# Performance work log

Hardware: AMD Instinct MI355X
Metric: run time of the kernel (lower is better)

The kernel has to match this reference:

```python
import jax, jax.numpy as jnp
import numpy as np

B, S_REF, E, H = 128, 2048, 512, 512

def setup_inputs() -> dict:
    key = jax.random.key(0)
    ks = jax.random.split(key, 13)
    def lin(kw, kb, out_d, in_d):
        bound = 1.0 / np.sqrt(in_d)
        w = jax.random.uniform(kw, (out_d, in_d), minval=-bound, maxval=bound, dtype=jnp.float32)
        b = jax.random.uniform(kb, (out_d,), minval=-bound, maxval=bound, dtype=jnp.float32)
        return w, b
    Wa_w, Wa_b = lin(ks[0], ks[1], H, H)
    Ua_w, Ua_b = lin(ks[2], ks[3], H, H)
    Va_w, Va_b = lin(ks[4], ks[5], 1, H)
    Wih_w, Wih_b = lin(ks[6], ks[7], H, E + H)
    Whh_w, Whh_b = lin(ks[8], ks[9], H, H)
    x_t = jax.random.normal(ks[10], (B, 1, E), dtype=jnp.float32)
    x_ref_encoded = jax.random.normal(ks[11], (B, S_REF, H), dtype=jnp.float32)
    h_prev = jax.random.normal(ks[12], (B, H), dtype=jnp.float32)
    return {"x_t": x_t, "x_ref_encoded": x_ref_encoded, "h_prev": h_prev,
            "Wa_w": Wa_w, "Wa_b": Wa_b, "Ua_w": Ua_w, "Ua_b": Ua_b,
            "Va_w": Va_w, "Va_b": Va_b, "Wih_w": Wih_w, "Wih_b": Wih_b,
            "Whh_w": Whh_w, "Whh_b": Whh_b}

def reference(x_t, x_ref_encoded, h_prev, Wa_w, Wa_b, Ua_w, Ua_b, Va_w, Va_b, Wih_w, Wih_b, Whh_w, Whh_b):
    # Bahdanau additive attention
    q = h_prev @ Wa_w.T + Wa_b                      # (B, H)
    k = jnp.einsum('bsh,oh->bso', x_ref_encoded, Ua_w) + Ua_b  # (B, S, H)
    scores = jnp.einsum('bsh,h->bs', jnp.tanh(q[:, None, :] + k), Va_w[0]) + Va_b[0]  # (B, S)
    attn_weights = jax.nn.softmax(scores, axis=1)
    context = jnp.einsum('bs,bsh->bh', attn_weights, x_ref_encoded)  # (B, H)
    # Reservoir RNN cell on concat(x_t[:,0,:], context)
    rnn_in = jnp.concatenate([x_t[:, 0, :], context], axis=1)        # (B, E+H)
    h_next = jnp.tanh(rnn_in @ Wih_w.T + Wih_b + h_prev @ Whh_w.T + Whh_b)
    return (h_next, context)
```

## Files before the change

### kernel.cpp

```cpp
#include <hip/hip_runtime.h>
#include <hip/hip_bf16.h>
#include <math.h>


typedef __attribute__((ext_vector_type(8))) short short8;
typedef __attribute__((ext_vector_type(8))) unsigned short ushort8;
typedef __attribute__((ext_vector_type(4))) float f32x4;

#define S_LEN 2048
#define BDIM 128
#define HDIM 512
#define EDIM 512
#define BM 64
#define NCHUNK (S_LEN / BM)

__device__ __forceinline__ unsigned short f2bf(float f) {
  unsigned int u = __float_as_uint(f);
  u += 0x7fffu + ((u >> 16) & 1u);
  return (unsigned short)(u >> 16);
}

__device__ __forceinline__ float bf2f(unsigned short u) {
  return __uint_as_float(((unsigned int)u) << 16);
}

__device__ __forceinline__ float fast_tanh(float x) {
  float e = __expf(2.0f * x);
  return 1.0f - 2.0f / (e + 1.0f);
}

__global__ __launch_bounds__(256) void k_cvt_b(const float* __restrict__ src,
                                               unsigned short* __restrict__ dst) {
  int tid = blockIdx.x * 256 + threadIdx.x;
  int ct = tid >> 10;
  int kt = (tid >> 6) & 15;
  int l = tid & 63;
  int col = ct * 16 + (l & 15);
  int k = kt * 32 + (l >> 4) * 8;
  const float4* s = (const float4*)(src + (size_t)col * HDIM + k);
  float4 v0 = s[0], v1 = s[1];
  ushort8 p;
  p[0] = f2bf(v0.x); p[1] = f2bf(v0.y); p[2] = f2bf(v0.z); p[3] = f2bf(v0.w);
  p[4] = f2bf(v1.x); p[5] = f2bf(v1.y); p[6] = f2bf(v1.z); p[7] = f2bf(v1.w);
  *(ushort8*)(dst + (size_t)tid * 8) = p;
}

__global__ __launch_bounds__(256) void k_q(const float* __restrict__ hp,
                                           const float* __restrict__ Wa,
                                           const float* __restrict__ Wab,
                                           const float* __restrict__ Uab,
                                           float* __restrict__ q) {
  int b = blockIdx.x, oh = blockIdx.y;
  int o = oh * 256 + threadIdx.x;
  __shared__ float hs[HDIM];
  hs[threadIdx.x] = hp[b * HDIM + threadIdx.x];
  hs[threadIdx.x + 256] = hp[b * HDIM + threadIdx.x + 256];
  __syncthreads();
  const float4* wr = (const float4*)(Wa + (size_t)o * HDIM);
  float acc = 0.f;
#pragma unroll 8
  for (int i = 0; i < HDIM / 4; ++i) {
    float4 v = wr[i];
    acc += v.x * hs[i * 4 + 0] + v.y * hs[i * 4 + 1] + v.z * hs[i * 4 + 2] + v.w * hs[i * 4 + 3];
  }
  q[b * HDIM + o] = acc + Wab[o] + Uab[o];
}

__global__ __launch_bounds__(512, 4) void k_scores_ctx(
    const float* __restrict__ xref, const unsigned short* __restrict__ uab,
    const float* __restrict__ q, const float* __restrict__ va,
    float* __restrict__ mArr, float* __restrict__ lArr, float* __restrict__ cpart) {
  int chunk = blockIdx.x;
  int b = blockIdx.y;
  int tid = threadIdx.x;
  int l = tid & 63;
  int w = tid >> 6;
  int c = l & 15, g4 = l >> 4;

  __shared__ __align__(16) unsigned short As[BM * HDIM];
  __shared__ float sc[BM];
  __shared__ float pl[BM];

  f32x4 acc[4][2];
#pragma unroll
  for (int m = 0; m < 4; ++m)
#pragma unroll
    for (int n = 0; n < 2; ++n) acc[m][n] = f32x4{0.f, 0.f, 0.f, 0.f};

  const float* xb = xref + ((size_t)b * S_LEN + (size_t)chunk * BM) * HDIM;

  int srow = tid >> 3;
  int sk8 = (tid & 7) * 64;
  int sw = (srow & 7) << 4;
  char* wbase = (char*)&As[0] + srow * 1024;
  float4 ga0, ga1, ga2, ga3, gb0, gb1, gb2, gb3;

#define ISSUE(v0, v1, v2, v3, call)                                            \
  {                                                                            \
    const float4* gp_ = (const float4*)(xb + (size_t)srow * HDIM + sk8 + (call) * 16); \
    v0 = gp_[0]; v1 = gp_[1]; v2 = gp_[2]; v3 = gp_[3];                        \
  }

#define WRITE(v0, v1, v2, v3, call)                                            \
  {                                                                            \
    union { __hip_bfloat162 h[4]; ushort8 s; } u0_, u1_;                       \
    u0_.h[0] = __float22bfloat162_rn(make_float2(v0.x, v0.y));                 \
    u0_.h[1] = __float22bfloat162_rn(make_float2(v0.z, v0.w));                 \
    u0_.h[2] = __float22bfloat162_rn(make_float2(v1.x, v1.y));                 \
    u0_.h[3] = __float22bfloat162_rn(make_float2(v1.z, v1.w));                 \
    u1_.h[0] = __float22bfloat162_rn(make_float2(v2.x, v2.y));                 \
    u1_.h[1] = __float22bfloat162_rn(make_float2(v2.z, v2.w));                 \
    u1_.h[2] = __float22bfloat162_rn(make_float2(v3.x, v3.y));                 \
    u1_.h[3] = __float22bfloat162_rn(make_float2(v3.z, v3.w));                 \
    int kb0_ = (tid & 7) * 128 + (call) * 32;                                  \
    *(ushort8*)(wbase + (kb0_ ^ sw)) = u0_.s;                                  \
    *(ushort8*)(wbase + ((kb0_ + 16) ^ sw)) = u1_.s;                           \
  }

#define CLUSTER(h, kt)                                                         \
  {                                                                            \
    short8 afr_[4], bfr_[2];                                                   \
    _Pragma("unroll")                                                          \
    for (int n = 0; n < 2; ++n) {                                              \
      int ct = (h) * 16 + w * 2 + n;                                           \
      bfr_[n] = *(const short8*)(uab + (((size_t)(ct * 16 + (kt)) * 64 + l) * 8)); \
    }                                                                          \
    _Pragma("unroll")                                                          \
    for (int m = 0; m < 4; ++m) {                                              \
      int row = m * 16 + (l & 15);                                             \
      int kb = ((kt) * 64 + (l >> 4) * 16) ^ ((row & 7) << 4);                 \
      afr_[m] = *(const short8*)((const char*)&As[0] + row * 1024 + kb);       \
    }                                                                          \
    __builtin_amdgcn_s_setprio(1);                                             \
    _Pragma("unroll")                                                          \
    for (int m = 0; m < 4; ++m)                                                \
      _Pragma("unroll")                                                        \
      for (int n = 0; n < 2; ++n)                                              \
        acc[m][n] = __builtin_amdgcn_mfma_f32_16x16x32_bf16(afr_[m], bfr_[n],  \
                                                            acc[m][n], 0, 0, 0); \
    __builtin_amdgcn_s_setprio(0);                                             \
  }

#define EPILOGUE(qf0_, qf1_, vf0_, vf1_)                                       \
  {                                                                            \
    _Pragma("unroll")                                                          \
    for (int m = 0; m < 4; ++m) {                                              \
      _Pragma("unroll")                                                        \
      for (int r = 0; r < 4; ++r) {                                            \
        float sum = fast_tanh(acc[m][0][r] + qf0_) * vf0_ +                    \
                    fast_tanh(acc[m][1][r] + qf1_) * vf1_;                     \
        sum += __shfl_xor(sum, 1);                                             \
        sum += __shfl_xor(sum, 2);                                             \
        sum += __shfl_xor(sum, 4);                                             \
        sum += __shfl_xor(sum, 8);                                             \
        if (c == 0) atomicAdd(&sc[m * 16 + g4 * 4 + r], sum);                  \
      }                                                                        \
    }                                                                          \
  }

  ISSUE(ga0, ga1, ga2, ga3, 0); ISSUE(gb0, gb1, gb2, gb3, 1);
  WRITE(ga0, ga1, ga2, ga3, 0); ISSUE(ga0, ga1, ga2, ga3, 2);
  WRITE(gb0, gb1, gb2, gb3, 1); ISSUE(gb0, gb1, gb2, gb3, 3);
  WRITE(ga0, ga1, ga2, ga3, 2); WRITE(gb0, gb1, gb2, gb3, 3);
  if (tid < BM) sc[tid] = 0.f;
  __syncthreads();

  {
    int o0 = w * 32 + c, o1 = w * 32 + 16 + c;
    float qf0 = q[b * HDIM + o0], qf1 = q[b * HDIM + o1];
    float vf0 = va[o0], vf1 = va[o1];
    CLUSTER(0, 0)  CLUSTER(0, 1)  CLUSTER(0, 2)  CLUSTER(0, 3)
    CLUSTER(0, 4)  CLUSTER(0, 5)  CLUSTER(0, 6)  CLUSTER(0, 7)
    CLUSTER(0, 8)  CLUSTER(0, 9)  CLUSTER(0, 10) CLUSTER(0, 11)
    CLUSTER(0, 12) CLUSTER(0, 13) CLUSTER(0, 14) CLUSTER(0, 15)
    EPILOGUE(qf0, qf1, vf0, vf1)
  }

#pragma unroll
  for (int m = 0; m < 4; ++m)
#pragma unroll
    for (int n = 0; n < 2; ++n) acc[m][n] = f32x4{0.f, 0.f, 0.f, 0.f};

  {
    int o0 = 256 + w * 32 + c, o1 = 256 + w * 32 + 16 + c;
    float qf0 = q[b * HDIM + o0], qf1 = q[b * HDIM + o1];
    float vf0 = va[o0], vf1 = va[o1];
    CLUSTER(1, 0)  CLUSTER(1, 1)  CLUSTER(1, 2)  CLUSTER(1, 3)
    CLUSTER(1, 4)  CLUSTER(1, 5)  CLUSTER(1, 6)  CLUSTER(1, 7)
    CLUSTER(1, 8)  CLUSTER(1, 9)  CLUSTER(1, 10) CLUSTER(1, 11)
    CLUSTER(1, 12) CLUSTER(1, 13) CLUSTER(1, 14) CLUSTER(1, 15)
    EPILOGUE(qf0, qf1, vf0, vf1)
  }
  __syncthreads();

  float M = sc[l];
#pragma unroll
  for (int off = 32; off >= 1; off >>= 1) M = fmaxf(M, __shfl_xor(M, off));
  float pp = __expf(sc[l] - M);
  float lsum = pp;
#pragma unroll
  for (int off = 32; off >= 1; off >>= 1) lsum += __shfl_xor(lsum, off);
  if (tid < BM) pl[tid] = pp;
  if (tid == 0) {
    mArr[b * NCHUNK + chunk] = M;
    lArr[b * NCHUNK + chunk] = lsum;
  }
  __syncthreads();

  {
    int h2 = tid * 2;
    const char* base_ = (const char*)&As[0];
    float cacc = 0.f;
#pragma unroll 8
    for (int r = 0; r < BM; ++r) {
      int byte = r * 1024 + (h2 ^ ((r & 7) << 4));
      cacc += pl[r] * bf2f(*(const unsigned short*)(base_ + byte));
    }
    cpart[((size_t)b * NCHUNK + chunk) * HDIM + tid] = cacc;
  }
#undef ISSUE
#undef WRITE
#undef CLUSTER
#undef EPILOGUE
}

__global__ __launch_bounds__(512) void k_combine(const float* __restrict__ mArr,
                                                 const float* __restrict__ lArr,
                                                 const float* __restrict__ cpart,
                                                 float* __restrict__ ctx,
                                                 float* __restrict__ out_ctx) {
  int b = blockIdx.x, t = threadIdx.x;
  __shared__ float wf[NCHUNK];
  __shared__ float dinv;
  if (t == 0) {
    float M = mArr[b * NCHUNK];
    for (int i = 1; i < NCHUNK; ++i) M = fmaxf(M, mArr[b * NCHUNK + i]);
    float den = 0.f;
    for (int i = 0; i < NCHUNK; ++i) {
      float f = __expf(mArr[b * NCHUNK + i] - M);
      wf[i] = f;
      den += f * lArr[b * NCHUNK + i];
    }
    dinv = 1.0f / den;
  }
  __syncthreads();
  float s = 0.f;
#pragma unroll
  for (int i = 0; i < NCHUNK; ++i) s += wf[i] * cpart[((size_t)b * NCHUNK + i) * HDIM + t];
  float c = s * dinv;
  ctx[b * HDIM + t] = c;
  out_ctx[b * HDIM + t] = c;
}

__global__ __launch_bounds__(256) void k_rnn(const float* __restrict__ xt,
                                             const float* __restrict__ ctx,
                                             const float* __restrict__ hp,
                                             const float* __restrict__ Wih,
                                             const float* __restrict__ Wihb,
                                             const float* __restrict__ Whh,
                                             const float* __restrict__ Whhb,
                                             float* __restrict__ hout) {
  int b = blockIdx.x, oh = blockIdx.y;
  int o = oh * 256 + threadIdx.x;
  __shared__ float xs[EDIM], cs[HDIM], hs[HDIM];
  xs[threadIdx.x] = xt[b * EDIM + threadIdx.x];
  xs[threadIdx.x + 256] = xt[b * EDIM + threadIdx.x + 256];
  cs[threadIdx.x] = ctx[b * HDIM + threadIdx.x];
  cs[threadIdx.x + 256] = ctx[b * HDIM + threadIdx.x + 256];
  hs[threadIdx.x] = hp[b * HDIM + threadIdx.x];
  hs[threadIdx.x + 256] = hp[b * HDIM + threadIdx.x + 256];
  __syncthreads();
  const float4* wi = (const float4*)(Wih + (size_t)o * (EDIM + HDIM));
  float acc = Wihb[o] + Whhb[o];
#pragma unroll 8
  for (int i = 0; i < EDIM / 4; ++i) {
    float4 v = wi[i];
    acc += v.x * xs[i * 4] + v.y * xs[i * 4 + 1] + v.z * xs[i * 4 + 2] + v.w * xs[i * 4 + 3];
  }
  const float4* wi2 = wi + EDIM / 4;
#pragma unroll 8
  for (int i = 0; i < HDIM / 4; ++i) {
    float4 v = wi2[i];
    acc += v.x * cs[i * 4] + v.y * cs[i * 4 + 1] + v.z * cs[i * 4 + 2] + v.w * cs[i * 4 + 3];
  }
  const float4* wh = (const float4*)(Whh + (size_t)o * HDIM);
#pragma unroll 8
  for (int i = 0; i < HDIM / 4; ++i) {
    float4 v = wh[i];
    acc += v.x * hs[i * 4] + v.y * hs[i * 4 + 1] + v.z * hs[i * 4 + 2] + v.w * hs[i * 4 + 3];
  }
  hout[b * HDIM + o] = tanhf(acc);
}

extern "C" void kernel_launch(void* const* d_in, const int* in_sizes, int n_in,
                              void* d_out, int out_size, void* d_ws, size_t ws_size,
                              hipStream_t stream) {
  const float* x_t    = (const float*)d_in[0];
  const float* x_ref  = (const float*)d_in[1];
  const float* h_prev = (const float*)d_in[2];
  const float* Wa_w   = (const float*)d_in[3];
  const float* Wa_b   = (const float*)d_in[4];
  const float* Ua_w   = (const float*)d_in[5];
  const float* Ua_b   = (const float*)d_in[6];
  const float* Va_w   = (const float*)d_in[7];
  const float* Wih_w  = (const float*)d_in[9];
  const float* Wih_b  = (const float*)d_in[10];
  const float* Whh_w  = (const float*)d_in[11];
  const float* Whh_b  = (const float*)d_in[12];

  char* ws = (char*)d_ws;
  unsigned short* ua_fr = (unsigned short*)ws;
  float* q     = (float*)(ws + 524288);
  float* mArr  = (float*)(ws + 786432);
  float* lArr  = (float*)(ws + 802816);
  float* cpart = (float*)(ws + 819200);
  float* ctx   = (float*)(ws + 9207808);

  float* h_out   = (float*)d_out;
  float* ctx_out = h_out + BDIM * HDIM;

  k_cvt_b<<<dim3(128), dim3(256), 0, stream>>>(Ua_w, ua_fr);
  k_q<<<dim3(BDIM, 2), dim3(256), 0, stream>>>(h_prev, Wa_w, Wa_b, Ua_b, q);
  k_scores_ctx<<<dim3(NCHUNK, BDIM), dim3(512), 0, stream>>>(x_ref, ua_fr, q, Va_w, mArr, lArr, cpart);
  k_combine<<<dim3(BDIM), dim3(512), 0, stream>>>(mArr, lArr, cpart, ctx, ctx_out);
  k_rnn<<<dim3(BDIM, 2), dim3(256), 0, stream>>>(x_t, ctx, h_prev, Wih_w, Wih_b, Whh_w, Whh_b, h_out);
}
```

Before: 350.4 us.

## Widen MFMA N-tile to four per wave and single-pass score epilogue

Result: faster. 294.9 us (-15.8%).

```diff
diff --git a/kernel.cpp b/kernel.cpp
--- a/kernel.cpp
+++ b/kernel.cpp
@@ -81,48 +81,42 @@
   __shared__ float sc[BM];
   __shared__ float pl[BM];
 
-  f32x4 acc[4][2];
+  f32x4 acc[4][4];
 #pragma unroll
   for (int m = 0; m < 4; ++m)
 #pragma unroll
-    for (int n = 0; n < 2; ++n) acc[m][n] = f32x4{0.f, 0.f, 0.f, 0.f};
+    for (int n = 0; n < 4; ++n) acc[m][n] = f32x4{0.f, 0.f, 0.f, 0.f};
 
   const float* xb = xref + ((size_t)b * S_LEN + (size_t)chunk * BM) * HDIM;
 
-  int srow = tid >> 3;
-  int sk8 = (tid & 7) * 64;
-  int sw = (srow & 7) << 4;
-  char* wbase = (char*)&As[0] + srow * 1024;
-  float4 ga0, ga1, ga2, ga3, gb0, gb1, gb2, gb3;
-
-#define ISSUE(v0, v1, v2, v3, call)                                            \
+  int srow = tid >> 3, skq = tid & 7;
+  char* wb = (char*)&As[0] + srow * 1024 + ((skq * 16) ^ ((srow & 7) << 4));
+  const float* sb = xb + (size_t)srow * HDIM + skq * 8;
+
+  float4 a0, a1, a2, a3, a4, a5, a6, a7;
+
+#define LD2(va, vb, p)                                                         \
   {                                                                            \
-    const float4* gp_ = (const float4*)(xb + (size_t)srow * HDIM + sk8 + (call) * 16); \
-    v0 = gp_[0]; v1 = gp_[1]; v2 = gp_[2]; v3 = gp_[3];                        \
-  }
-
-#define WRITE(v0, v1, v2, v3, call)                                            \
+    va = *(const float4*)(sb + (p) * 64);                                      \
+    vb = *(const float4*)(sb + (p) * 64 + 4);                                  \
+  }
+
+#define WR1(va, vb, p)                                                         \
   {                                                                            \
-    union { __hip_bfloat162 h[4]; ushort8 s; } u0_, u1_;                       \
-    u0_.h[0] = __float22bfloat162_rn(make_float2(v0.x, v0.y));                 \
-    u0_.h[1] = __float22bfloat162_rn(make_float2(v0.z, v0.w));                 \
-    u0_.h[2] = __float22bfloat162_rn(make_float2(v1.x, v1.y));                 \
-    u0_.h[3] = __float22bfloat162_rn(make_float2(v1.z, v1.w));                 \
-    u1_.h[0] = __float22bfloat162_rn(make_float2(v2.x, v2.y));                 \
-    u1_.h[1] = __float22bfloat162_rn(make_float2(v2.z, v2.w));                 \
-    u1_.h[2] = __float22bfloat162_rn(make_float2(v3.x, v3.y));                 \
-    u1_.h[3] = __float22bfloat162_rn(make_float2(v3.z, v3.w));                 \
-    int kb0_ = (tid & 7) * 128 + (call) * 32;                                  \
-    *(ushort8*)(wbase + (kb0_ ^ sw)) = u0_.s;                                  \
-    *(ushort8*)(wbase + ((kb0_ + 16) ^ sw)) = u1_.s;                           \
-  }
-
-#define CLUSTER(h, kt)                                                         \
+    union { __hip_bfloat162 h[4]; ushort8 s; } u_;                             \
+    u_.h[0] = __float22bfloat162_rn(make_float2(va.x, va.y));                  \
+    u_.h[1] = __float22bfloat162_rn(make_float2(va.z, va.w));                  \
+    u_.h[2] = __float22bfloat162_rn(make_float2(vb.x, vb.y));                  \
+    u_.h[3] = __float22bfloat162_rn(make_float2(vb.z, vb.w));                  \
+    *(ushort8*)(wb + (p) * 128) = u_.s;                                        \
+  }
+
+#define CLUSTER(kt)                                                            \
   {                                                                            \
-    short8 afr_[4], bfr_[2];                                                   \
+    short8 afr_[4], bfr_[4];                                                   \
     _Pragma("unroll")                                                          \
-    for (int n = 0; n < 2; ++n) {                                              \
-      int ct = (h) * 16 + w * 2 + n;                                           \
+    for (int n = 0; n < 4; ++n) {                                              \
+      int ct = w * 4 + n;                                                      \
       bfr_[n] = *(const short8*)(uab + (((size_t)(ct * 16 + (kt)) * 64 + l) * 8)); \
     }                                                                          \
     _Pragma("unroll")                                                          \
@@ -135,61 +129,46 @@
     _Pragma("unroll")                                                          \
     for (int m = 0; m < 4; ++m)                                                \
       _Pragma("unroll")                                                        \
-      for (int n = 0; n < 2; ++n)                                              \
+      for (int n = 0; n < 4; ++n)                                              \
         acc[m][n] = __builtin_amdgcn_mfma_f32_16x16x32_bf16(afr_[m], bfr_[n],  \
                                                             acc[m][n], 0, 0, 0); \
     __builtin_amdgcn_s_setprio(0);                                             \
   }
 
-#define EPILOGUE(qf0_, qf1_, vf0_, vf1_)                                       \
-  {                                                                            \
-    _Pragma("unroll")                                                          \
-    for (int m = 0; m < 4; ++m) {                                              \
-      _Pragma("unroll")                                                        \
-      for (int r = 0; r < 4; ++r) {                                            \
-        float sum = fast_tanh(acc[m][0][r] + qf0_) * vf0_ +                    \
-                    fast_tanh(acc[m][1][r] + qf1_) * vf1_;                     \
-        sum += __shfl_xor(sum, 1);                                             \
-        sum += __shfl_xor(sum, 2);                                             \
-        sum += __shfl_xor(sum, 4);                                             \
-        sum += __shfl_xor(sum, 8);                                             \
-        if (c == 0) atomicAdd(&sc[m * 16 + g4 * 4 + r], sum);                  \
-      }                                                                        \
-    }                                                                          \
-  }
-
-  ISSUE(ga0, ga1, ga2, ga3, 0); ISSUE(gb0, gb1, gb2, gb3, 1);
-  WRITE(ga0, ga1, ga2, ga3, 0); ISSUE(ga0, ga1, ga2, ga3, 2);
-  WRITE(gb0, gb1, gb2, gb3, 1); ISSUE(gb0, gb1, gb2, gb3, 3);
-  WRITE(ga0, ga1, ga2, ga3, 2); WRITE(gb0, gb1, gb2, gb3, 3);
+  LD2(a0, a1, 0) LD2(a2, a3, 1) LD2(a4, a5, 2) LD2(a6, a7, 3)
+  WR1(a0, a1, 0) WR1(a2, a3, 1) WR1(a4, a5, 2) WR1(a6, a7, 3)
+  LD2(a0, a1, 4) LD2(a2, a3, 5) LD2(a4, a5, 6) LD2(a6, a7, 7)
+  WR1(a0, a1, 4) WR1(a2, a3, 5) WR1(a4, a5, 6) WR1(a6, a7, 7)
   if (tid < BM) sc[tid] = 0.f;
   __syncthreads();
 
-  {
-    int o0 = w * 32 + c, o1 = w * 32 + 16 + c;
-    float qf0 = q[b * HDIM + o0], qf1 = q[b * HDIM + o1];
-    float vf0 = va[o0], vf1 = va[o1];
-    CLUSTER(0, 0)  CLUSTER(0, 1)  CLUSTER(0, 2)  CLUSTER(0, 3)
-    CLUSTER(0, 4)  CLUSTER(0, 5)  CLUSTER(0, 6)  CLUSTER(0, 7)
-    CLUSTER(0, 8)  CLUSTER(0, 9)  CLUSTER(0, 10) CLUSTER(0, 11)
-    CLUSTER(0, 12) CLUSTER(0, 13) CLUSTER(0, 14) CLUSTER(0, 15)
-    EPILOGUE(qf0, qf1, vf0, vf1)
-  }
-
-#pragma unroll
-  for (int m = 0; m < 4; ++m)
-#pragma unroll
-    for (int n = 0; n < 2; ++n) acc[m][n] = f32x4{0.f, 0.f, 0.f, 0.f};
-
-  {
-    int o0 = 256 + w * 32 + c, o1 = 256 + w * 32 + 16 + c;
-    float qf0 = q[b * HDIM + o0], qf1 = q[b * HDIM + o1];
-    float vf0 = va[o0], vf1 = va[o1];
-    CLUSTER(1, 0)  CLUSTER(1, 1)  CLUSTER(1, 2)  CLUSTER(1, 3)
-    CLUSTER(1, 4)  CLUSTER(1, 5)  CLUSTER(1, 6)  CLUSTER(1, 7)
-    CLUSTER(1, 8)  CLUSTER(1, 9)  CLUSTER(1, 10) CLUSTER(1, 11)
-    CLUSTER(1, 12) CLUSTER(1, 13) CLUSTER(1, 14) CLUSTER(1, 15)
-    EPILOGUE(qf0, qf1, vf0, vf1)
+  CLUSTER(0)  CLUSTER(1)  CLUSTER(2)  CLUSTER(3)
+  CLUSTER(4)  CLUSTER(5)  CLUSTER(6)  CLUSTER(7)
+  CLUSTER(8)  CLUSTER(9)  CLUSTER(10) CLUSTER(11)
+  CLUSTER(12) CLUSTER(13)
+
+  float qf[4], vf[4];
+#pragma unroll
+  for (int n = 0; n < 4; ++n) {
+    int o = w * 64 + n * 16 + c;
+    qf[n] = q[b * HDIM + o];
+    vf[n] = va[o];
+  }
+  CLUSTER(14) CLUSTER(15)
+
+#pragma unroll
+  for (int m = 0; m < 4; ++m) {
+#pragma unroll
+    for (int r = 0; r < 4; ++r) {
+      float sum = 0.f;
+#pragma unroll
+      for (int n = 0; n < 4; ++n) sum += fast_tanh(acc[m][n][r] + qf[n]) * vf[n];
+      sum += __shfl_xor(sum, 1);
+      sum += __shfl_xor(sum, 2);
+      sum += __shfl_xor(sum, 4);
+      sum += __shfl_xor(sum, 8);
+      if (c == 0) atomicAdd(&sc[m * 16 + g4 * 4 + r], sum);
+    }
   }
   __syncthreads();
 
@@ -218,10 +197,9 @@
     }
     cpart[((size_t)b * NCHUNK + chunk) * HDIM + tid] = cacc;
   }
-#undef ISSUE
-#undef WRITE
+#undef LD2
+#undef WR1
 #undef CLUSTER
-#undef EPILOGUE
 }
 
 __global__ __launch_bounds__(512) void k_combine(const float* __restrict__ mArr,
```
